# Kernel tuning notes

Measured on AMD Instinct MI355X. Metric: run time of the kernel, lower is better.

Reference implementation:

```python
import jax, jax.numpy as jnp
import numpy as np

N = 50000      # nodes
E = 800000     # edges (avg degree 16)
F_IN = 3       # dataset.num_node_features
H = 256        # hidden_channels
G = 64         # batch_size (num graphs)
OUT = 24       # lin_out output dim


def setup_inputs() -> dict:
    key = jax.random.key(0)
    ks = jax.random.split(key, 16)
    s = 0.05
    inp = {
        "x": jax.random.normal(ks[0], (N, F_IN), jnp.float32),
        "edge_index": jax.random.randint(ks[1], (2, E), 0, N, dtype=jnp.int32),
        "batch": jnp.sort(jax.random.randint(ks[2], (N,), 0, G, dtype=jnp.int32)),
        # layer 1 (F_IN -> H)
        "w_rel1": jax.random.normal(ks[3], (F_IN, H), jnp.float32) * s,
        "w_root1": jax.random.normal(ks[4], (F_IN, H), jnp.float32) * s,
        "b1": jnp.zeros((H,), jnp.float32),
        # layers 2..7 (H -> H), stacked
        "w_rel": jax.random.normal(ks[5], (6, H, H), jnp.float32) * s,
        "w_root": jax.random.normal(ks[6], (6, H, H), jnp.float32) * s,
        "b": jnp.zeros((6, H), jnp.float32),
        # output head
        "w_out": jax.random.normal(ks[7], (H, OUT), jnp.float32) * s,
        "b_out": jnp.zeros((OUT,), jnp.float32),
    }
    return inp


def reference(x, edge_index, batch, w_rel1, w_root1, b1, w_rel, w_root, b, w_out, b_out):
    src, dst = edge_index[0], edge_index[1]

    def conv(h, wr, wro, bb):
        # PyG GraphConv with add aggregation:
        # out_i = W_rel @ sum_{j -> i} h_j + b + W_root @ h_i
        agg = jax.ops.segment_sum(h[src], dst, num_segments=N)
        return agg @ wr + h @ wro + bb

    h = jax.nn.relu(conv(x, w_rel1, w_root1, b1))
    for i in range(6):
        h = jax.nn.relu(conv(h, w_rel[i], w_root[i], b[i]))

    # global_mean_pool over batch segment ids
    counts = jax.ops.segment_sum(jnp.ones((N,), h.dtype), batch, num_segments=G)
    pooled = jax.ops.segment_sum(h, batch, num_segments=G) / jnp.maximum(counts, 1.0)[:, None]

    # dropout is identity in eval mode
    return pooled @ w_out + b_out
```

## Files before the change

kernel.cpp:

```cpp
#include <hip/hip_runtime.h>

#define N_NODES 50000
#define MPAD 50048
#define N_EDGES 800000
#define F_INPUT 3
#define H 256
#define K_CAT 512
#define G_BATCH 64
#define OUT_DIM 24

#define SCAN_BLK 256
#define NBLK ((N_NODES + SCAN_BLK - 1) / SCAN_BLK)

typedef __attribute__((ext_vector_type(8))) short short8;
typedef __attribute__((ext_vector_type(4))) float float4v;

__device__ __forceinline__ float bf2f(unsigned short u) {
    return __uint_as_float(((unsigned)u) << 16);
}
__device__ __forceinline__ unsigned short f2bf(float f) {
    unsigned x = __float_as_uint(f);
    unsigned r = (x + 0x7FFFu + ((x >> 16) & 1u)) >> 16;
    return (unsigned short)r;
}

__device__ __forceinline__ void async_copy16(void* lds, const void* g) {
    __builtin_amdgcn_global_load_lds(
        (const __attribute__((address_space(1))) unsigned int*)g,
        (__attribute__((address_space(3))) unsigned int*)lds, 16, 0, 0);
}


__global__ void histo_kernel(const int* __restrict__ dst, int* __restrict__ deg,
                             int* __restrict__ epos) {
    int e = blockIdx.x * blockDim.x + threadIdx.x;
    if (e < N_EDGES) epos[e] = atomicAdd(&deg[dst[e]], 1);
}

__global__ void scan_block(int* __restrict__ deg, int* __restrict__ rowptr,
                           int* __restrict__ blockSums) {
    __shared__ int s[SCAN_BLK];
    int idx = blockIdx.x * SCAN_BLK + threadIdx.x;
    int v = (idx < N_NODES) ? deg[idx] : 0;
    s[threadIdx.x] = v;
    __syncthreads();
    for (int off = 1; off < SCAN_BLK; off <<= 1) {
        int t = (threadIdx.x >= off) ? s[threadIdx.x - off] : 0;
        __syncthreads();
        s[threadIdx.x] += t;
        __syncthreads();
    }
    if (idx < N_NODES) {
        rowptr[idx] = s[threadIdx.x] - v;
        deg[idx] = 0;
    }
    if (threadIdx.x == SCAN_BLK - 1) blockSums[blockIdx.x] = s[threadIdx.x];
}

__global__ void scan_sums(int* __restrict__ blockSums, int* __restrict__ rowptr) {
    __shared__ int s[SCAN_BLK];
    int v = (threadIdx.x < NBLK) ? blockSums[threadIdx.x] : 0;
    s[threadIdx.x] = v;
    __syncthreads();
    for (int off = 1; off < SCAN_BLK; off <<= 1) {
        int t = (threadIdx.x >= off) ? s[threadIdx.x - off] : 0;
        __syncthreads();
        s[threadIdx.x] += t;
        __syncthreads();
    }
    if (threadIdx.x < NBLK) blockSums[threadIdx.x] = s[threadIdx.x] - v;
    if (threadIdx.x == SCAN_BLK - 1) rowptr[N_NODES] = s[threadIdx.x];
}

__global__ void scan_add(int* __restrict__ rowptr, const int* __restrict__ blockSums) {
    int idx = blockIdx.x * blockDim.x + threadIdx.x;
    if (idx < N_NODES) rowptr[idx] += blockSums[idx >> 8];
}

__global__ void fill_csr(const int* __restrict__ src, const int* __restrict__ dst,
                         const int* __restrict__ rowptr, const int* __restrict__ epos,
                         int* __restrict__ csr_src) {
    int e = blockIdx.x * blockDim.x + threadIdx.x;
    if (e >= N_EDGES) return;
    csr_src[rowptr[dst[e]] + epos[e]] = src[e];
}


__global__ void prep_weights(const float* __restrict__ w_rel, const float* __restrict__ w_root,
                             unsigned short* __restrict__ WcatT) {
    int idx = blockIdx.x * blockDim.x + threadIdx.x;
    if (idx >= 6 * K_CAT * H) return;
    int n = idx & (H - 1);
    int k = (idx >> 8) & (K_CAT - 1);
    int l = idx >> 17;
    float v = (k < H) ? w_rel[(size_t)l * H * H + k * H + n]
                      : w_root[(size_t)l * H * H + (k - H) * H + n];
    WcatT[(size_t)l * H * K_CAT + (size_t)n * K_CAT + k] = f2bf(v);
}


__global__ void agg3(const float* __restrict__ x, const int* __restrict__ rowptr,
                     const int* __restrict__ csr_src, float* __restrict__ agg) {
    int n = blockIdx.x * blockDim.x + threadIdx.x;
    if (n >= N_NODES) return;
    int beg = rowptr[n], end = rowptr[n + 1];
    float a0 = 0.f, a1 = 0.f, a2 = 0.f;
    for (int i = beg; i < end; ++i) {
        int s = csr_src[i];
        a0 += x[s * 3 + 0];
        a1 += x[s * 3 + 1];
        a2 += x[s * 3 + 2];
    }
    agg[n * 3 + 0] = a0;
    agg[n * 3 + 1] = a1;
    agg[n * 3 + 2] = a2;
}

__global__ void layer1_kernel(const float* __restrict__ x, const float* __restrict__ agg,
                              const float* __restrict__ wr, const float* __restrict__ wro,
                              const float* __restrict__ bias, unsigned short* __restrict__ cat) {
    int n = blockIdx.x;
    int f = threadIdx.x;
    float a0 = agg[n * 3 + 0], a1 = agg[n * 3 + 1], a2 = agg[n * 3 + 2];
    float x0 = x[n * 3 + 0], x1 = x[n * 3 + 1], x2 = x[n * 3 + 2];
    float v = bias[f];
    v += a0 * wr[0 * H + f] + a1 * wr[1 * H + f] + a2 * wr[2 * H + f];
    v += x0 * wro[0 * H + f] + x1 * wro[1 * H + f] + x2 * wro[2 * H + f];
    cat[(size_t)n * K_CAT + H + f] = f2bf(fmaxf(v, 0.f));
}


__global__ __launch_bounds__(256) void quantH(const unsigned short* __restrict__ cat,
                                              unsigned char* __restrict__ h8,
                                              float* __restrict__ hscale) {
    int gtid = blockIdx.x * blockDim.x + threadIdx.x;
    int node = gtid >> 6;
    if (node >= N_NODES) return;
    int lane = threadIdx.x & 63;
    const unsigned short* hrow = cat + (size_t)node * K_CAT + H;
    uint2 v = *(const uint2*)(hrow + lane * 4);
    float f0 = __uint_as_float(v.x << 16);
    float f1 = __uint_as_float(v.x & 0xffff0000u);
    float f2 = __uint_as_float(v.y << 16);
    float f3 = __uint_as_float(v.y & 0xffff0000u);
    float m = fmaxf(fmaxf(f0, f1), fmaxf(f2, f3));
#pragma unroll
    for (int off = 1; off < 64; off <<= 1)
        m = fmaxf(m, __shfl_xor(m, off, 64));
    m = fmaxf(m, 1e-30f);
    float inv = 255.f / m;
    unsigned q0 = (unsigned)(int)rintf(f0 * inv);
    unsigned q1 = (unsigned)(int)rintf(f1 * inv);
    unsigned q2 = (unsigned)(int)rintf(f2 * inv);
    unsigned q3 = (unsigned)(int)rintf(f3 * inv);
    unsigned packed = q0 | (q1 << 8) | (q2 << 16) | (q3 << 24);
    *(unsigned*)(h8 + (size_t)node * H + lane * 4) = packed;
    if (lane == 0) hscale[node] = m / 255.f;
}


__global__ __launch_bounds__(256) void aggH(unsigned short* __restrict__ cat,
                                            const unsigned char* __restrict__ h8,
                                            const float* __restrict__ hscale,
                                            const int* __restrict__ rowptr,
                                            const int* __restrict__ csr_src) {
    int gtid = blockIdx.x * blockDim.x + threadIdx.x;
    int node = gtid >> 6;
    if (node >= N_NODES) return;
    int lane = threadIdx.x & 63;
    int sub = lane >> 4;
    int fl = lane & 15;
    int beg = rowptr[node], end = rowptr[node + 1];
    float acc[16] = {};
    const unsigned char* base = h8 + fl * 16;

    for (int i = beg; i < end; i += 4) {
        int idx = i + sub;
        int clamped = idx < end ? idx : end - 1;
        int s = csr_src[clamped];
        float sc = (idx < end) ? hscale[s] : 0.f;
        uint4 q = *(const uint4*)(base + (size_t)s * H);
        acc[0]  = fmaf((float)(q.x & 0xffu), sc, acc[0]);
        acc[1]  = fmaf((float)((q.x >> 8) & 0xffu), sc, acc[1]);
        acc[2]  = fmaf((float)((q.x >> 16) & 0xffu), sc, acc[2]);
        acc[3]  = fmaf((float)(q.x >> 24), sc, acc[3]);
        acc[4]  = fmaf((float)(q.y & 0xffu), sc, acc[4]);
        acc[5]  = fmaf((float)((q.y >> 8) & 0xffu), sc, acc[5]);
        acc[6]  = fmaf((float)((q.y >> 16) & 0xffu), sc, acc[6]);
        acc[7]  = fmaf((float)(q.y >> 24), sc, acc[7]);
        acc[8]  = fmaf((float)(q.z & 0xffu), sc, acc[8]);
        acc[9]  = fmaf((float)((q.z >> 8) & 0xffu), sc, acc[9]);
        acc[10] = fmaf((float)((q.z >> 16) & 0xffu), sc, acc[10]);
        acc[11] = fmaf((float)(q.z >> 24), sc, acc[11]);
        acc[12] = fmaf((float)(q.w & 0xffu), sc, acc[12]);
        acc[13] = fmaf((float)((q.w >> 8) & 0xffu), sc, acc[13]);
        acc[14] = fmaf((float)((q.w >> 16) & 0xffu), sc, acc[14]);
        acc[15] = fmaf((float)(q.w >> 24), sc, acc[15]);
    }

#pragma unroll
    for (int j = 0; j < 16; j++) {
        acc[j] += __shfl_xor(acc[j], 16, 64);
        acc[j] += __shfl_xor(acc[j], 32, 64);
    }

    if (sub == 0) {
        unsigned short* o = cat + (size_t)node * K_CAT + fl * 16;
        uint4 p0, p1;
        p0.x = (unsigned)f2bf(acc[0])  | ((unsigned)f2bf(acc[1]) << 16);
        p0.y = (unsigned)f2bf(acc[2])  | ((unsigned)f2bf(acc[3]) << 16);
        p0.z = (unsigned)f2bf(acc[4])  | ((unsigned)f2bf(acc[5]) << 16);
        p0.w = (unsigned)f2bf(acc[6])  | ((unsigned)f2bf(acc[7]) << 16);
        p1.x = (unsigned)f2bf(acc[8])  | ((unsigned)f2bf(acc[9]) << 16);
        p1.y = (unsigned)f2bf(acc[10]) | ((unsigned)f2bf(acc[11]) << 16);
        p1.z = (unsigned)f2bf(acc[12]) | ((unsigned)f2bf(acc[13]) << 16);
        p1.w = (unsigned)f2bf(acc[14]) | ((unsigned)f2bf(acc[15]) << 16);
        *(uint4*)o = p0;
        *(uint4*)(o + 8) = p1;
    }
}


#define GBM 128
#define GBN 128
#define GBK 64

__global__ __launch_bounds__(256) void gemm_mfma(
    const unsigned short* __restrict__ cat, const unsigned short* __restrict__ WcatT,
    const float* __restrict__ bias, unsigned short* __restrict__ catOut) {
    __shared__ unsigned short sA[GBM][GBK];
    __shared__ unsigned short sB[GBN][GBK];

    const int tid = threadIdx.x;
    const int wave = tid >> 6;
    const int lane = tid & 63;
    const int quad = lane >> 4;
    const int l16 = lane & 15;
    const int wm0 = (wave & 1) * 64;
    const int wn0 = (wave >> 1) * 64;
    const int m0 = blockIdx.x * GBM;
    const int n0 = blockIdx.y * GBN;

    const int rowoff = lane >> 3;
    const int schunk = ((lane & 7) ^ rowoff) * 8;
    const unsigned short* Asrc[4];
    const unsigned short* Bsrc[4];
#pragma unroll
    for (int j = 0; j < 4; j++) {
        int q = wave * 4 + j;
        Asrc[j] = cat + (size_t)(m0 + q * 8 + rowoff) * K_CAT + schunk;
        Bsrc[j] = WcatT + (size_t)(n0 + q * 8 + rowoff) * K_CAT + schunk;
    }

    const int sw = l16 & 7;
    const int ca0 = (quad ^ sw) * 8;
    const int ca1 = ((4 + quad) ^ sw) * 8;

    float4v acc[4][4] = {};

    for (int kk = 0; kk < K_CAT; kk += GBK) {
#pragma unroll
        for (int j = 0; j < 4; j++) {
            char* da = (char*)sA + (wave * 4 + j) * 1024;
            char* db = (char*)sB + (wave * 4 + j) * 1024;
            async_copy16(da, Asrc[j] + kk);
            async_copy16(db, Bsrc[j] + kk);
        }
        __syncthreads();

        short8 a[4][2], b[4][2];
#pragma unroll
        for (int i = 0; i < 4; i++) {
            const unsigned short* ra = &sA[wm0 + i * 16 + l16][0];
            const unsigned short* rb = &sB[wn0 + i * 16 + l16][0];
            a[i][0] = *(const short8*)(ra + ca0);
            a[i][1] = *(const short8*)(ra + ca1);
            b[i][0] = *(const short8*)(rb + ca0);
            b[i][1] = *(const short8*)(rb + ca1);
        }
#pragma unroll
        for (int sub = 0; sub < 2; sub++)
#pragma unroll
            for (int mi = 0; mi < 4; mi++)
#pragma unroll
                for (int ni = 0; ni < 4; ni++)
                    acc[mi][ni] = __builtin_amdgcn_mfma_f32_16x16x32_bf16(
                        a[mi][sub], b[ni][sub], acc[mi][ni], 0, 0, 0);
        __syncthreads();
    }

#pragma unroll
    for (int ni = 0; ni < 4; ni++) {
        int col = n0 + wn0 + ni * 16 + l16;
        float bc = bias[col];
#pragma unroll
        for (int mi = 0; mi < 4; mi++) {
            int row = m0 + wm0 + mi * 16 + quad * 4;
#pragma unroll
            for (int r = 0; r < 4; r++) {
                float v = acc[mi][ni][r] + bc;
                catOut[(size_t)(row + r) * K_CAT + H + col] = f2bf(fmaxf(v, 0.f));
            }
        }
    }
}


__device__ __forceinline__ int lowerBound(const int* __restrict__ batch, int val) {
    int lo = 0, hi = N_NODES;
    while (lo < hi) {
        int mid = (lo + hi) >> 1;
        if (batch[mid] < val) lo = mid + 1; else hi = mid;
    }
    return lo;
}

__global__ void pool_partial(const unsigned short* __restrict__ cat, const int* __restrict__ batch,
                             float* __restrict__ pooled) {
    int g = blockIdx.x;
    int seg = blockIdx.y;
    int f = threadIdx.x;
    int start = lowerBound(batch, g);
    int end = lowerBound(batch, g + 1);
    int len = end - start;
    int s0 = start + (int)((long long)len * seg / 8);
    int s1 = start + (int)((long long)len * (seg + 1) / 8);
    float sum = 0.f;
    for (int n = s0; n < s1; ++n)
        sum += bf2f(cat[(size_t)n * K_CAT + H + f]);
    if (s1 > s0)
        atomicAdd(&pooled[g * H + f], sum);
}

__global__ void head_kernel(const float* __restrict__ pooled, const int* __restrict__ batch,
                            const float* __restrict__ w_out, const float* __restrict__ b_out,
                            float* __restrict__ out) {
    int g = blockIdx.x;
    int o = threadIdx.x;
    int start = lowerBound(batch, g);
    int end = lowerBound(batch, g + 1);
    float cnt = fmaxf((float)(end - start), 1.f);
    float sum = 0.f;
    for (int f = 0; f < H; ++f)
        sum += pooled[g * H + f] * w_out[f * OUT_DIM + o];
    out[g * OUT_DIM + o] = b_out[o] + sum / cnt;
}


extern "C" void kernel_launch(void* const* d_in, const int* in_sizes, int n_in,
                              void* d_out, int out_size, void* d_ws, size_t ws_size,
                              hipStream_t stream) {
    const float* x      = (const float*)d_in[0];
    const int*   ei     = (const int*)d_in[1];
    const int*   batch  = (const int*)d_in[2];
    const float* w_rel1 = (const float*)d_in[3];
    const float* w_root1= (const float*)d_in[4];
    const float* b1     = (const float*)d_in[5];
    const float* w_rel  = (const float*)d_in[6];
    const float* w_root = (const float*)d_in[7];
    const float* b      = (const float*)d_in[8];
    const float* w_out  = (const float*)d_in[9];
    const float* b_out  = (const float*)d_in[10];
    float* out = (float*)d_out;

    const int* src = ei;
    const int* dst = ei + N_EDGES;

    unsigned short* catA  = (unsigned short*)d_ws;
    unsigned short* catB  = catA + (size_t)MPAD * K_CAT;
    unsigned short* WcatT = catB + (size_t)MPAD * K_CAT;
    float* agg3buf = (float*)(WcatT + (size_t)6 * H * K_CAT);
    float* pooled  = agg3buf + (size_t)N_NODES * 4;
    float* hscale  = pooled + G_BATCH * H;
    int* rowptr    = (int*)(hscale + N_NODES);
    int* degcur    = rowptr + (N_NODES + 1);
    int* blockSums = degcur + N_NODES;
    int* csr_src   = blockSums + SCAN_BLK;
    int* epos      = csr_src + N_EDGES;
    unsigned char* h8 = (unsigned char*)(epos + N_EDGES);

    hipMemsetAsync(degcur, 0, N_NODES * sizeof(int), stream);
    histo_kernel<<<(N_EDGES + 255) / 256, 256, 0, stream>>>(dst, degcur, epos);
    scan_block<<<NBLK, SCAN_BLK, 0, stream>>>(degcur, rowptr, blockSums);
    scan_sums<<<1, SCAN_BLK, 0, stream>>>(blockSums, rowptr);
    scan_add<<<NBLK, SCAN_BLK, 0, stream>>>(rowptr, blockSums);
    fill_csr<<<(N_EDGES + 255) / 256, 256, 0, stream>>>(src, dst, rowptr, epos, csr_src);

    prep_weights<<<(6 * K_CAT * H + 255) / 256, 256, 0, stream>>>(w_rel, w_root, WcatT);

    agg3<<<(N_NODES + 255) / 256, 256, 0, stream>>>(x, rowptr, csr_src, agg3buf);
    layer1_kernel<<<N_NODES, H, 0, stream>>>(x, agg3buf, w_rel1, w_root1, b1, catA);

    unsigned short* cur = catA;
    unsigned short* nxt = catB;
    for (int l = 0; l < 6; ++l) {
        quantH<<<(N_NODES * 64 + 255) / 256, 256, 0, stream>>>(cur, h8, hscale);
        aggH<<<(N_NODES * 64 + 255) / 256, 256, 0, stream>>>(cur, h8, hscale, rowptr, csr_src);
        dim3 grid(MPAD / GBM, H / GBN);
        gemm_mfma<<<grid, 256, 0, stream>>>(cur, WcatT + (size_t)l * H * K_CAT,
                                            b + (size_t)l * H, nxt);
        unsigned short* t = cur; cur = nxt; nxt = t;
    }

    hipMemsetAsync(pooled, 0, G_BATCH * H * sizeof(float), stream);
    pool_partial<<<dim3(G_BATCH, 8), 256, 0, stream>>>(cur, batch, pooled);
    head_kernel<<<G_BATCH, OUT_DIM, 0, stream>>>(pooled, batch, w_out, b_out, out);
}
```

Before: 684.3 us.

## Fuse int8 quantization into GEMM/layer1 epilogues with per-64-column scales, prefetch aggH

Removes the separate quantH pass by quantizing activations to int8 directly in the layer-1 kernel and the MFMA GEMM epilogue. Each node now gets four scales, one per 64-column group, and a permuted byte layout matches the GEMM output lanes. To compensate, the w_rel rows are permuted in prep_weights so the aggregated features line up. aggH gains software prefetch of the next edge's index, scale and payload, plus an early exit for zero-degree nodes. The two scan tail kernels are merged into one. The aim is to save one full read and write of the activations per layer and some launch overhead, at the cost of a more complex GEMM epilogue with shuffles and extra stores.

```diff
diff --git a/kernel.cpp b/kernel.cpp
--- a/kernel.cpp
+++ b/kernel.cpp
@@ -3,7 +3,6 @@
 #define N_NODES 50000
 #define MPAD 50048
 #define N_EDGES 800000
-#define F_INPUT 3
 #define H 256
 #define K_CAT 512
 #define G_BATCH 64
@@ -31,13 +30,14 @@
 }
 
 
+
 __global__ void histo_kernel(const int* __restrict__ dst, int* __restrict__ deg,
                              int* __restrict__ epos) {
     int e = blockIdx.x * blockDim.x + threadIdx.x;
     if (e < N_EDGES) epos[e] = atomicAdd(&deg[dst[e]], 1);
 }
 
-__global__ void scan_block(int* __restrict__ deg, int* __restrict__ rowptr,
+__global__ void scan_block(const int* __restrict__ deg, int* __restrict__ rowptr,
                            int* __restrict__ blockSums) {
     __shared__ int s[SCAN_BLK];
     int idx = blockIdx.x * SCAN_BLK + threadIdx.x;
@@ -50,31 +50,26 @@
         s[threadIdx.x] += t;
         __syncthreads();
     }
-    if (idx < N_NODES) {
-        rowptr[idx] = s[threadIdx.x] - v;
-        deg[idx] = 0;
-    }
+    if (idx < N_NODES) rowptr[idx] = s[threadIdx.x] - v;
     if (threadIdx.x == SCAN_BLK - 1) blockSums[blockIdx.x] = s[threadIdx.x];
 }
 
-__global__ void scan_sums(int* __restrict__ blockSums, int* __restrict__ rowptr) {
+__global__ void scan_finish(int* __restrict__ rowptr, const int* __restrict__ blockSums) {
     __shared__ int s[SCAN_BLK];
-    int v = (threadIdx.x < NBLK) ? blockSums[threadIdx.x] : 0;
-    s[threadIdx.x] = v;
+    int t = threadIdx.x;
+    int v = (t < NBLK) ? blockSums[t] : 0;
+    s[t] = v;
     __syncthreads();
     for (int off = 1; off < SCAN_BLK; off <<= 1) {
-        int t = (threadIdx.x >= off) ? s[threadIdx.x - off] : 0;
-        __syncthreads();
-        s[threadIdx.x] += t;
-        __syncthreads();
-    }
-    if (threadIdx.x < NBLK) blockSums[threadIdx.x] = s[threadIdx.x] - v;
-    if (threadIdx.x == SCAN_BLK - 1) rowptr[N_NODES] = s[threadIdx.x];
-}
-
-__global__ void scan_add(int* __restrict__ rowptr, const int* __restrict__ blockSums) {
-    int idx = blockIdx.x * blockDim.x + threadIdx.x;
-    if (idx < N_NODES) rowptr[idx] += blockSums[idx >> 8];
+        int tv = (t >= off) ? s[t - off] : 0;
+        __syncthreads();
+        s[t] += tv;
+        __syncthreads();
+    }
+    int prefix = (blockIdx.x > 0) ? s[blockIdx.x - 1] : 0;
+    int idx = blockIdx.x * SCAN_BLK + t;
+    if (idx < N_NODES) rowptr[idx] += prefix;
+    if (blockIdx.x == 0 && t == 0) rowptr[N_NODES] = s[NBLK - 1];
 }
 
 __global__ void fill_csr(const int* __restrict__ src, const int* __restrict__ dst,
@@ -93,8 +88,13 @@
     int n = idx & (H - 1);
     int k = (idx >> 8) & (K_CAT - 1);
     int l = idx >> 17;
-    float v = (k < H) ? w_rel[(size_t)l * H * H + k * H + n]
-                      : w_root[(size_t)l * H * H + (k - H) * H + n];
+    float v;
+    if (k < H) {
+        int f = (k & 0xC0) | ((k & 3) << 4) | ((k >> 2) & 15);
+        v = w_rel[(size_t)l * H * H + f * H + n];
+    } else {
+        v = w_root[(size_t)l * H * H + (k - H) * H + n];
+    }
     WcatT[(size_t)l * H * K_CAT + (size_t)n * K_CAT + k] = f2bf(v);
 }
 
@@ -118,7 +118,9 @@
 
 __global__ void layer1_kernel(const float* __restrict__ x, const float* __restrict__ agg,
                               const float* __restrict__ wr, const float* __restrict__ wro,
-                              const float* __restrict__ bias, unsigned short* __restrict__ cat) {
+                              const float* __restrict__ bias, unsigned short* __restrict__ cat,
+                              unsigned char* __restrict__ h8, float* __restrict__ hscale) {
+    __shared__ unsigned char tmp[H];
     int n = blockIdx.x;
     int f = threadIdx.x;
     float a0 = agg[n * 3 + 0], a1 = agg[n * 3 + 1], a2 = agg[n * 3 + 2];
@@ -126,36 +128,16 @@
     float v = bias[f];
     v += a0 * wr[0 * H + f] + a1 * wr[1 * H + f] + a2 * wr[2 * H + f];
     v += x0 * wro[0 * H + f] + x1 * wro[1 * H + f] + x2 * wro[2 * H + f];
-    cat[(size_t)n * K_CAT + H + f] = f2bf(fmaxf(v, 0.f));
-}
-
-
-__global__ __launch_bounds__(256) void quantH(const unsigned short* __restrict__ cat,
-                                              unsigned char* __restrict__ h8,
-                                              float* __restrict__ hscale) {
-    int gtid = blockIdx.x * blockDim.x + threadIdx.x;
-    int node = gtid >> 6;
-    if (node >= N_NODES) return;
-    int lane = threadIdx.x & 63;
-    const unsigned short* hrow = cat + (size_t)node * K_CAT + H;
-    uint2 v = *(const uint2*)(hrow + lane * 4);
-    float f0 = __uint_as_float(v.x << 16);
-    float f1 = __uint_as_float(v.x & 0xffff0000u);
-    float f2 = __uint_as_float(v.y << 16);
-    float f3 = __uint_as_float(v.y & 0xffff0000u);
-    float m = fmaxf(fmaxf(f0, f1), fmaxf(f2, f3));
-#pragma unroll
-    for (int off = 1; off < 64; off <<= 1)
-        m = fmaxf(m, __shfl_xor(m, off, 64));
-    m = fmaxf(m, 1e-30f);
-    float inv = 255.f / m;
-    unsigned q0 = (unsigned)(int)rintf(f0 * inv);
-    unsigned q1 = (unsigned)(int)rintf(f1 * inv);
-    unsigned q2 = (unsigned)(int)rintf(f2 * inv);
-    unsigned q3 = (unsigned)(int)rintf(f3 * inv);
-    unsigned packed = q0 | (q1 << 8) | (q2 << 16) | (q3 << 24);
-    *(unsigned*)(h8 + (size_t)node * H + lane * 4) = packed;
-    if (lane == 0) hscale[node] = m / 255.f;
+    v = fmaxf(v, 0.f);
+    cat[(size_t)n * K_CAT + H + f] = f2bf(v);
+    float m = v;
+#pragma unroll
+    for (int off = 1; off < 64; off <<= 1) m = fmaxf(m, __shfl_xor(m, off, 64));
+    float inv = m > 0.f ? 255.f / m : 0.f;
+    tmp[(f & 0xC0) | ((f & 15) << 2) | ((f >> 4) & 3)] = (unsigned char)(v * inv + 0.5f);
+    if ((f & 63) == 0) hscale[n * 4 + (f >> 6)] = m * (1.f / 255.f);
+    __syncthreads();
+    if (f < 64) *(unsigned*)(h8 + (size_t)n * H + f * 4) = *(const unsigned*)(tmp + f * 4);
 }
 
 
@@ -170,32 +152,59 @@
     int lane = threadIdx.x & 63;
     int sub = lane >> 4;
     int fl = lane & 15;
+    int g = fl >> 2;
     int beg = rowptr[node], end = rowptr[node + 1];
+
+    if (beg >= end) {
+        if (sub == 0) {
+            uint4 z = make_uint4(0, 0, 0, 0);
+            unsigned short* o = cat + (size_t)node * K_CAT + fl * 16;
+            *(uint4*)o = z;
+            *(uint4*)(o + 8) = z;
+        }
+        return;
+    }
+
     float acc[16] = {};
     const unsigned char* base = h8 + fl * 16;
+    int last = end - 1;
+
+    int ia = beg + sub;
+    int ca = ia < end ? ia : last;
+    int sa = csr_src[ca];
+    int ib = beg + 4 + sub;
+    int cb = ib < end ? ib : last;
+    int sb = csr_src[cb];
+    float sca = (ia < end) ? hscale[sa * 4 + g] : 0.f;
+    uint4 qa = *(const uint4*)(base + (size_t)sa * H);
 
     for (int i = beg; i < end; i += 4) {
-        int idx = i + sub;
-        int clamped = idx < end ? idx : end - 1;
-        int s = csr_src[clamped];
-        float sc = (idx < end) ? hscale[s] : 0.f;
-        uint4 q = *(const uint4*)(base + (size_t)s * H);
-        acc[0]  = fmaf((float)(q.x & 0xffu), sc, acc[0]);
-        acc[1]  = fmaf((float)((q.x >> 8) & 0xffu), sc, acc[1]);
-        acc[2]  = fmaf((float)((q.x >> 16) & 0xffu), sc, acc[2]);
-        acc[3]  = fmaf((float)(q.x >> 24), sc, acc[3]);
-        acc[4]  = fmaf((float)(q.y & 0xffu), sc, acc[4]);
-        acc[5]  = fmaf((float)((q.y >> 8) & 0xffu), sc, acc[5]);
-        acc[6]  = fmaf((float)((q.y >> 16) & 0xffu), sc, acc[6]);
-        acc[7]  = fmaf((float)(q.y >> 24), sc, acc[7]);
-        acc[8]  = fmaf((float)(q.z & 0xffu), sc, acc[8]);
-        acc[9]  = fmaf((float)((q.z >> 8) & 0xffu), sc, acc[9]);
-        acc[10] = fmaf((float)((q.z >> 16) & 0xffu), sc, acc[10]);
-        acc[11] = fmaf((float)(q.z >> 24), sc, acc[11]);
-        acc[12] = fmaf((float)(q.w & 0xffu), sc, acc[12]);
-        acc[13] = fmaf((float)((q.w >> 8) & 0xffu), sc, acc[13]);
-        acc[14] = fmaf((float)((q.w >> 16) & 0xffu), sc, acc[14]);
-        acc[15] = fmaf((float)(q.w >> 24), sc, acc[15]);
+        int ic = i + 8 + sub;
+        int cc = ic < end ? ic : last;
+        int sn = csr_src[cc];
+        int inb = i + 4 + sub;
+        float scb = (inb < end) ? hscale[sb * 4 + g] : 0.f;
+        uint4 qb = *(const uint4*)(base + (size_t)sb * H);
+
+        float sc = sca;
+        acc[0]  = fmaf((float)(qa.x & 0xffu), sc, acc[0]);
+        acc[1]  = fmaf((float)((qa.x >> 8) & 0xffu), sc, acc[1]);
+        acc[2]  = fmaf((float)((qa.x >> 16) & 0xffu), sc, acc[2]);
+        acc[3]  = fmaf((float)(qa.x >> 24), sc, acc[3]);
+        acc[4]  = fmaf((float)(qa.y & 0xffu), sc, acc[4]);
+        acc[5]  = fmaf((float)((qa.y >> 8) & 0xffu), sc, acc[5]);
+        acc[6]  = fmaf((float)((qa.y >> 16) & 0xffu), sc, acc[6]);
+        acc[7]  = fmaf((float)(qa.y >> 24), sc, acc[7]);
+        acc[8]  = fmaf((float)(qa.z & 0xffu), sc, acc[8]);
+        acc[9]  = fmaf((float)((qa.z >> 8) & 0xffu), sc, acc[9]);
+        acc[10] = fmaf((float)((qa.z >> 16) & 0xffu), sc, acc[10]);
+        acc[11] = fmaf((float)(qa.z >> 24), sc, acc[11]);
+        acc[12] = fmaf((float)(qa.w & 0xffu), sc, acc[12]);
+        acc[13] = fmaf((float)((qa.w >> 8) & 0xffu), sc, acc[13]);
+        acc[14] = fmaf((float)((qa.w >> 16) & 0xffu), sc, acc[14]);
+        acc[15] = fmaf((float)(qa.w >> 24), sc, acc[15]);
+
+        sa = sb; sb = sn; sca = scb; qa = qb;
     }
 
 #pragma unroll
@@ -227,7 +236,8 @@
 
 __global__ __launch_bounds__(256) void gemm_mfma(
     const unsigned short* __restrict__ cat, const unsigned short* __restrict__ WcatT,
-    const float* __restrict__ bias, unsigned short* __restrict__ catOut) {
+    const float* __restrict__ bias, unsigned short* __restrict__ catOut,
+    unsigned char* __restrict__ h8, float* __restrict__ hscale) {
     __shared__ unsigned short sA[GBM][GBK];
     __shared__ unsigned short sB[GBN][GBK];
 
@@ -289,18 +299,39 @@
         __syncthreads();
     }
 
-#pragma unroll
-    for (int ni = 0; ni < 4; ni++) {
-        int col = n0 + wn0 + ni * 16 + l16;
-        float bc = bias[col];
-#pragma unroll
-        for (int mi = 0; mi < 4; mi++) {
-            int row = m0 + wm0 + mi * 16 + quad * 4;
-#pragma unroll
-            for (int r = 0; r < 4; r++) {
-                float v = acc[mi][ni][r] + bc;
-                catOut[(size_t)(row + r) * K_CAT + H + col] = f2bf(fmaxf(v, 0.f));
-            }
+    const int hb = n0 + wn0 + l16 * 4;
+    const int gsc = (n0 + wn0) >> 6;
+    float bcol[4];
+#pragma unroll
+    for (int ni = 0; ni < 4; ni++) bcol[ni] = bias[n0 + wn0 + ni * 16 + l16];
+
+#pragma unroll
+    for (int mi = 0; mi < 4; mi++) {
+        int rowb = m0 + wm0 + mi * 16 + quad * 4;
+#pragma unroll
+        for (int r = 0; r < 4; r++) {
+            int row = rowb + r;
+            float v0 = fmaxf(acc[mi][0][r] + bcol[0], 0.f);
+            float v1 = fmaxf(acc[mi][1][r] + bcol[1], 0.f);
+            float v2 = fmaxf(acc[mi][2][r] + bcol[2], 0.f);
+            float v3 = fmaxf(acc[mi][3][r] + bcol[3], 0.f);
+            unsigned short* co = catOut + (size_t)row * K_CAT + H + n0 + wn0 + l16;
+            co[0]  = f2bf(v0);
+            co[16] = f2bf(v1);
+            co[32] = f2bf(v2);
+            co[48] = f2bf(v3);
+            float m = fmaxf(fmaxf(v0, v1), fmaxf(v2, v3));
+            m = fmaxf(m, __shfl_xor(m, 1, 64));
+            m = fmaxf(m, __shfl_xor(m, 2, 64));
+            m = fmaxf(m, __shfl_xor(m, 4, 64));
+            m = fmaxf(m, __shfl_xor(m, 8, 64));
+            float inv = m > 0.f ? 255.f / m : 0.f;
+            unsigned p = (unsigned)(v0 * inv + 0.5f)
+                       | ((unsigned)(v1 * inv + 0.5f) << 8)
+                       | ((unsigned)(v2 * inv + 0.5f) << 16)
+                       | ((unsigned)(v3 * inv + 0.5f) << 24);
+            *(unsigned*)(h8 + (size_t)row * H + hb) = p;
+            if (l16 == 0) hscale[row * 4 + gsc] = m * (1.f / 255.f);
         }
     }
 }
@@ -372,7 +403,7 @@
     float* agg3buf = (float*)(WcatT + (size_t)6 * H * K_CAT);
     float* pooled  = agg3buf + (size_t)N_NODES * 4;
     float* hscale  = pooled + G_BATCH * H;
-    int* rowptr    = (int*)(hscale + N_NODES);
+    int* rowptr    = (int*)(hscale + (size_t)MPAD * 4);
     int* degcur    = rowptr + (N_NODES + 1);
     int* blockSums = degcur + N_NODES;
     int* csr_src   = blockSums + SCAN_BLK;
@@ -382,23 +413,21 @@
     hipMemsetAsync(degcur, 0, N_NODES * sizeof(int), stream);
     histo_kernel<<<(N_EDGES + 255) / 256, 256, 0, stream>>>(dst, degcur, epos);
     scan_block<<<NBLK, SCAN_BLK, 0, stream>>>(degcur, rowptr, blockSums);
-    scan_sums<<<1, SCAN_BLK, 0, stream>>>(blockSums, rowptr);
-    scan_add<<<NBLK, SCAN_BLK, 0, stream>>>(rowptr, blockSums);
+    scan_finish<<<NBLK, SCAN_BLK, 0, stream>>>(rowptr, blockSums);
     fill_csr<<<(N_EDGES + 255) / 256, 256, 0, stream>>>(src, dst, rowptr, epos, csr_src);
 
     prep_weights<<<(6 * K_CAT * H + 255) / 256, 256, 0, stream>>>(w_rel, w_root, WcatT);
 
     agg3<<<(N_NODES + 255) / 256, 256, 0, stream>>>(x, rowptr, csr_src, agg3buf);
-    layer1_kernel<<<N_NODES, H, 0, stream>>>(x, agg3buf, w_rel1, w_root1, b1, catA);
+    layer1_kernel<<<N_NODES, H, 0, stream>>>(x, agg3buf, w_rel1, w_root1, b1, catA, h8, hscale);
 
     unsigned short* cur = catA;
     unsigned short* nxt = catB;
     for (int l = 0; l < 6; ++l) {
-        quantH<<<(N_NODES * 64 + 255) / 256, 256, 0, stream>>>(cur, h8, hscale);
         aggH<<<(N_NODES * 64 + 255) / 256, 256, 0, stream>>>(cur, h8, hscale, rowptr, csr_src);
         dim3 grid(MPAD / GBM, H / GBN);
         gemm_mfma<<<grid, 256, 0, stream>>>(cur, WcatT + (size_t)l * H * K_CAT,
-                                            b + (size_t)l * H, nxt);
+                                            b + (size_t)l * H, nxt, h8, hscale);
         unsigned short* t = cur; cur = nxt; nxt = t;
     }
 
```

After: 680.0 us. About the same (-0.6%).
